# Optimization experiments

Measured on AMD Instinct MI355X. Metric: run time of the kernel, lower is better.

Reference implementation:

```python
import jax, jax.numpy as jnp
import numpy as np

B, T, D, K = 4, 2048, 1024, 4

def setup_inputs() -> dict:
    key = jax.random.key(0)
    ks = jax.random.split(key, 4)
    u = jax.random.normal(ks[0], (B, T, D), dtype=jnp.float32)
    s0 = jnp.zeros((B, K, D), dtype=jnp.float32)
    W_in = jax.random.normal(ks[1], (K * D, D), dtype=jnp.float32) * (1.0 / np.sqrt(D))
    b_in = jnp.zeros((K * D,), dtype=jnp.float32)
    W_out = jax.random.normal(ks[2], (D, K * D), dtype=jnp.float32) * (1.0 / np.sqrt(K * D))
    b_out = jnp.zeros((D,), dtype=jnp.float32)
    decay_logit = jax.random.normal(ks[3], (K,), dtype=jnp.float32)
    return {"u": u, "s0": s0, "W_in": W_in, "b_in": b_in,
            "W_out": W_out, "b_out": b_out, "decay_logit": decay_logit}

def reference(u, s0, W_in, b_in, W_out, b_out, decay_logit):
    # u: (B,T,D); s0: (B,K,D)
    Bb, Tt, Dd = u.shape
    Kk = decay_logit.shape[0]
    # input projection -> (B,T,K,D) -> (T,B,K,D) for scan over time
    inp = (jnp.einsum('btd,ed->bte', u, W_in) + b_in).reshape(Bb, Tt, Kk, Dd)
    xs = jnp.transpose(inp, (1, 0, 2, 3))  # (T,B,K,D)
    decay = jax.nn.sigmoid(decay_logit).reshape(1, Kk, 1)  # (1,K,1)

    def step(s, x):
        s_next = decay * s + x
        return s_next, s_next

    s_last, s_seq = jax.lax.scan(step, s0, xs)  # s_seq: (T,B,K,D)
    g_in = jnp.transpose(s_seq, (1, 0, 2, 3)).reshape(Bb, Tt, Kk * Dd)
    g = jnp.einsum('bte,de->btd', g_in, W_out) + b_out
    return g, s_last
```

## Files before the change

### kernel.cpp

```cpp
#include <hip/hip_runtime.h>


#define Bb 4
#define Tt 2048
#define Dd 1024
#define Kk 4
#define BT (Bb*Tt)
#define Ee (Kk*Dd)
#define NCH 32
#define LCH 64

typedef __bf16 bf16x8 __attribute__((ext_vector_type(8)));
typedef float  f32x4  __attribute__((ext_vector_type(4)));

__device__ __forceinline__ float bf2f(ushort u){
  union { unsigned int i; float f; } x; x.i = ((unsigned int)u) << 16; return x.f;
}
__device__ __forceinline__ ushort f2bf(float f){
  union { unsigned int i; float f; } x; x.f = f;
  unsigned int i = x.i;
  return (ushort)((i + 0x7FFFu + ((i >> 16) & 1u)) >> 16);
}
__device__ __forceinline__ float lo16(unsigned u){
  union { unsigned i; float f; } x; x.i = u << 16; return x.f;
}
__device__ __forceinline__ float hi16(unsigned u){
  union { unsigned i; float f; } x; x.i = u & 0xFFFF0000u; return x.f;
}
__device__ __forceinline__ float sigm(float x){ return 1.0f / (1.0f + expf(-x)); }

__global__ __launch_bounds__(256) void k_transpose(const float* __restrict__ in,
                                                   ushort* __restrict__ out){
  __shared__ float tile[32][33];
  int tx = threadIdx.x, ty = threadIdx.y;
  int c0 = blockIdx.x * 32, r0 = blockIdx.y * 32;
  #pragma unroll
  for (int j = 0; j < 4; ++j)
    tile[ty + j*8][tx] = in[(size_t)(r0 + ty + j*8) * Dd + c0 + tx];
  __syncthreads();
  #pragma unroll
  for (int j = 0; j < 4; ++j)
    out[(size_t)(c0 + ty + j*8) * Ee + r0 + tx] = f2bf(tile[tx][ty + j*8]);
}

__global__ __launch_bounds__(256) void k_wout(const float* __restrict__ Wout,
                                              const float* __restrict__ s0,
                                              const float* __restrict__ b_in,
                                              ushort* __restrict__ Wout_bf,
                                              float* __restrict__ z0,
                                              float* __restrict__ cterm){
  int gid  = blockIdx.x * 4 + (threadIdx.x >> 6);
  int lane = threadIdx.x & 63;
  int d = gid & 1023, k = gid >> 10;
  const float* wrow = Wout + (size_t)d * Ee + k * Dd;
  ushort*      wbf  = Wout_bf + (size_t)d * Ee + k * Dd;
  const float* bv   = b_in + k * Dd;
  float sc = 0.f, sz0 = 0.f, sz1 = 0.f, sz2 = 0.f, sz3 = 0.f;
  #pragma unroll
  for (int j = 0; j < 4; ++j){
    int base = lane*4 + j*256;
    float4 wv = *(const float4*)(wrow + base);
    ushort4 ob; ob.x = f2bf(wv.x); ob.y = f2bf(wv.y); ob.z = f2bf(wv.z); ob.w = f2bf(wv.w);
    *(ushort4*)(wbf + base) = ob;
    float4 bb = *(const float4*)(bv + base);
    sc += wv.x*bb.x + wv.y*bb.y + wv.z*bb.z + wv.w*bb.w;
    #pragma unroll
    for (int b = 0; b < 4; ++b){
      const float* sv = s0 + ((size_t)(b*Kk + k) << 10) + base;
      float4 s4 = *(const float4*)sv;
      float acc = wv.x*s4.x + wv.y*s4.y + wv.z*s4.z + wv.w*s4.w;
      if (b == 0) sz0 += acc; else if (b == 1) sz1 += acc;
      else if (b == 2) sz2 += acc; else sz3 += acc;
    }
  }
  for (int off = 32; off; off >>= 1){
    sc  += __shfl_down(sc, off);
    sz0 += __shfl_down(sz0, off);
    sz1 += __shfl_down(sz1, off);
    sz2 += __shfl_down(sz2, off);
    sz3 += __shfl_down(sz3, off);
  }
  if (lane == 0){
    cterm[gid] = sc;
    z0[gid]          = sz0;
    z0[gid + 4096]   = sz1;
    z0[gid + 8192]   = sz2;
    z0[gid + 12288]  = sz3;
  }
}

__global__ __launch_bounds__(256) void gemm_nt(const ushort* __restrict__ A,
                                               const ushort* __restrict__ B,
                                               ushort* __restrict__ C,
                                               int Kred, int lda, int ldb, int ldc,
                                               long aBatch, long bBatch, long cBatch){
  __shared__ ushort As[128 * 32];
  __shared__ ushort Bs[128 * 32];
  A += (long)blockIdx.z * aBatch;
  B += (long)blockIdx.z * bBatch;
  C += (long)blockIdx.z * cBatch;
  const int tid  = threadIdx.x;
  const int lane = tid & 63;
  const int w    = tid >> 6;
  const int wr   = w >> 1, wc = w & 1;
  const int rowBase = blockIdx.x * 128;
  const int colBase = blockIdx.y * 128;

  f32x4 acc[4][4] = {};
  const int krow = (lane >> 4) * 8;
  const int rsel = lane & 15;

  for (int kk = 0; kk < Kred; kk += 32){
    __syncthreads();
    #pragma unroll
    for (int i = 0; i < 2; ++i){
      int c  = i * 256 + tid;
      int r  = c >> 2;
      int c8 = (c & 3) * 8;
      const ushort* ga = A + (size_t)(rowBase + r) * lda + kk + c8;
      const ushort* gb = B + (size_t)(colBase + r) * ldb + kk + c8;
      __builtin_amdgcn_global_load_lds((const __attribute__((address_space(1))) void*)ga,
                                       (__attribute__((address_space(3))) void*)&As[c * 8],
                                       16, 0, 0);
      __builtin_amdgcn_global_load_lds((const __attribute__((address_space(1))) void*)gb,
                                       (__attribute__((address_space(3))) void*)&Bs[c * 8],
                                       16, 0, 0);
    }
    asm volatile("s_waitcnt vmcnt(0)" ::: "memory");
    __syncthreads();

    bf16x8 Af[4], Bf[4];
    #pragma unroll
    for (int mi = 0; mi < 4; ++mi)
      Af[mi] = *(const bf16x8*)&As[(wr*64 + mi*16 + rsel) * 32 + krow];
    #pragma unroll
    for (int ni = 0; ni < 4; ++ni)
      Bf[ni] = *(const bf16x8*)&Bs[(wc*64 + ni*16 + rsel) * 32 + krow];
    #pragma unroll
    for (int mi = 0; mi < 4; ++mi)
      #pragma unroll
      for (int ni = 0; ni < 4; ++ni)
        acc[mi][ni] = __builtin_amdgcn_mfma_f32_16x16x32_bf16(Af[mi], Bf[ni], acc[mi][ni], 0, 0, 0);
  }

  #pragma unroll
  for (int mi = 0; mi < 4; ++mi){
    #pragma unroll
    for (int ni = 0; ni < 4; ++ni){
      int r0 = rowBase + wr*64 + mi*16 + (lane >> 4) * 4;
      int c0 = colBase + wc*64 + ni*16 + (lane & 15);
      #pragma unroll
      for (int q = 0; q < 4; ++q)
        C[(size_t)(r0 + q) * ldc + c0] = f2bf(acc[mi][ni][q]);
    }
  }
}

#define STAGE_OP(GB, LOFF)                                                     \
  { _Pragma("unroll")                                                          \
    for (int i_ = 0; i_ < 2; ++i_){                                            \
      int c_ = tid + i_*256;                                                   \
      int row_ = c_ >> 2;                                                      \
      int ss_ = (c_ & 3) ^ ((row_ >> 1) & 3);                                  \
      const ushort* g_ = (GB) + (size_t)row_ * 1024 + ss_ * 8;                 \
      __builtin_amdgcn_global_load_lds(                                        \
        (const __attribute__((address_space(1))) void*)g_,                     \
        (__attribute__((address_space(3))) void*)&lds[(LOFF) + c_*8],          \
        16, 0, 0);                                                             \
    } }

#define LOAD_A4(DST)                                                           \
  { _Pragma("unroll")                                                          \
    for (int mi_ = 0; mi_ < 4; ++mi_){                                         \
      int r_ = wm*64 + mi_*16 + rsel;                                          \
      int uo_ = r_*32 + kq*8;                                                  \
      uo_ ^= ((uo_ >> 6) & 3) << 3;                                            \
      DST[mi_] = *(const bf16x8*)&lds[cbase + uo_];                            \
    } }

#define LOAD_B4(DST)                                                           \
  { _Pragma("unroll")                                                          \
    for (int ni_ = 0; ni_ < 4; ++ni_){                                         \
      int r_ = wn*64 + ni_*16 + rsel;                                          \
      int uo_ = r_*32 + kq*8;                                                  \
      uo_ ^= ((uo_ >> 6) & 3) << 3;                                            \
      DST[ni_] = *(const bf16x8*)&lds[cbase + 4096 + uo_];                     \
    } }

#define XB(R) ((((R) & 3) ^ (((R) >> 2) & 3)) << 5)
#define BAR() __builtin_amdgcn_s_barrier()

__global__ __launch_bounds__(256, 4) void gemm_big(const ushort* __restrict__ A,
                                                   const ushort* __restrict__ B,
                                                   ushort* __restrict__ C,
                                                   const float* __restrict__ dlog,
                                                   float* __restrict__ carry){
  __shared__ ushort lds[16384];
  const int tid  = threadIdx.x;
  const int lane = tid & 63;
  const int w    = tid >> 6;
  const int wm   = w >> 1;
  const int wn   = w & 1;
  const int rsel = lane & 15;
  const int kq   = lane >> 4;

  int bid = blockIdx.x;
  int xcd = bid & 7, rr = bid >> 3;
  const int rowBase = ((xcd >> 1) * 16 + (rr & 15)) * 128;
  const int colBase = ((xcd & 1) * 16 + (rr >> 4)) * 128;

  const ushort* Ag = A + (size_t)rowBase * 1024;
  const ushort* Bg = B + (size_t)colBase * 1024;

  f32x4 acc[4][4] = {};

  STAGE_OP(Ag +  0, 0);
  STAGE_OP(Bg +  0, 4096);
  STAGE_OP(Ag + 32, 8192);
  STAGE_OP(Bg + 32, 8192 + 4096);
  asm volatile("s_waitcnt vmcnt(4)" ::: "memory");
  BAR();

  for (int t = 0; t < 32; ++t){
    const int cbase = (t & 1) * 8192;
    bf16x8 af[4], bf[4];
    LOAD_A4(af); LOAD_B4(bf);
    #pragma unroll
    for (int mi = 0; mi < 4; ++mi)
      #pragma unroll
      for (int ni = 0; ni < 4; ++ni)
        acc[mi][ni] = __builtin_amdgcn_mfma_f32_16x16x32_bf16(af[mi], bf[ni], acc[mi][ni], 0, 0, 0);
    asm volatile("s_waitcnt lgkmcnt(0)" ::: "memory");
    BAR();
    if (t < 30){
      STAGE_OP(Ag + (t+2)*32, cbase);
      STAGE_OP(Bg + (t+2)*32, cbase + 4096);
      asm volatile("s_waitcnt vmcnt(4)" ::: "memory");
    } else {
      asm volatile("s_waitcnt vmcnt(0)" ::: "memory");
    }
    BAR();
  }

  #pragma unroll
  for (int mi = 0; mi < 4; ++mi){
    #pragma unroll
    for (int j = 0; j < 4; ++j){
      #pragma unroll
      for (int q = 0; q < 4; ++q){
        int row = wm*64 + mi*16 + (lane >> 4)*4 + q;
        int col = wn*64 + j*16 + rsel;
        int byte = (row*256 + col*2) ^ XB(row);
        *(ushort*)((char*)lds + byte) = f2bf(acc[mi][j][q]);
      }
    }
  }
  __syncthreads();

  if (tid < 128){
    const int k_blk = colBase >> 10;
    const int b_blk = rowBase >> 11;
    const int ch0   = (rowBase & 2047) >> 6;
    const int d0    = colBase & 1023;
    const float p   = sigm(dlog[k_blk]);
    int cp = tid & 63, ch = tid >> 6;
    float a0 = 0.f, a1 = 0.f;
    for (int i = 0; i < 64; ++i){
      int row = ch*64 + i;
      int byte = (row*256 + cp*4) ^ XB(row);
      unsigned v = *(const unsigned*)((char*)lds + byte);
      a0 = p * a0 + lo16(v);
      a1 = p * a1 + hi16(v);
    }
    float* cdst = &carry[(size_t)((b_blk*Kk + k_blk)*NCH + ch0 + ch) * Dd + d0 + cp*2];
    cdst[0] = a0; cdst[1] = a1;
  }

  #pragma unroll
  for (int j = 0; j < 8; ++j){
    int idx = tid + j*256;
    int r = idx >> 4, c16 = idx & 15;
    int byte = (r*256 + c16*16) ^ XB(r);
    f32x4 v = *(const f32x4*)((char*)lds + byte);
    *(f32x4*)&C[(size_t)(rowBase + r) * Ee + colBase + c16*8] = v;
  }
}

__global__ __launch_bounds__(256) void k_scanInc(const float* __restrict__ carry,
                                                 const float* __restrict__ z0,
                                                 const float* __restrict__ dlog,
                                                 float* __restrict__ incoming){
  int idx = blockIdx.x * 256 + threadIdx.x;
  int k = (idx >> 10) & 3;
  int bk = idx >> 10, d = idx & 1023;
  float p  = sigm(dlog[k]);
  float dL = powf(p, (float)LCH);
  float inc = z0[idx];
  for (int c = 0; c < NCH; ++c){
    size_t o = ((size_t)(bk * NCH + c)) * Dd + d;
    incoming[o] = inc;
    inc = dL * inc + carry[o];
  }
}

__global__ __launch_bounds__(256) void k_scanB(const ushort* __restrict__ Y,
                                               const float* __restrict__ incoming,
                                               const float* __restrict__ dlog,
                                               const float* __restrict__ b_out,
                                               const float* __restrict__ cterm,
                                               float* __restrict__ g){
  int x = blockIdx.x;
  int d = blockIdx.y * 256 + threadIdx.x;
  int c = x & 31, b = x >> 5;
  float p[4], z[4], ct[4], pw[4];
  #pragma unroll
  for (int k = 0; k < 4; ++k){
    p[k]  = sigm(dlog[k]);
    z[k]  = incoming[((size_t)(((b*Kk + k))*NCH + c)) * Dd + d];
    float omp = fmaxf(1.0f - p[k], 1e-30f);
    ct[k] = cterm[k * Dd + d] / omp;
    pw[k] = powf(p[k], (float)(c * LCH + 1));
  }
  float bo = b_out[d];
  size_t ybase = ((size_t)(b*Tt + c*LCH)) * Ee + d;
  size_t gbase = ((size_t)(b*Tt + c*LCH)) * Dd + d;
  for (int i = 0; i < LCH; ++i){
    float acc = bo;
    #pragma unroll
    for (int k = 0; k < 4; ++k){
      z[k] = p[k] * z[k] + bf2f(Y[ybase + (size_t)k * Dd]);
      acc += z[k] + ct[k] * (1.0f - pw[k]);
      pw[k] *= p[k];
    }
    g[gbase] = acc;
    ybase += Ee; gbase += Dd;
  }
}

__global__ __launch_bounds__(256) void k_prep(const float* __restrict__ u,
                                              const float* __restrict__ dlog,
                                              float* __restrict__ vpart,
                                              ushort* __restrict__ U_bf){
  int x = blockIdx.x;
  int d = blockIdx.y * 256 + threadIdx.x;
  int c = x & 31, b = x >> 5;
  float p[4], a[4] = {0.f, 0.f, 0.f, 0.f};
  #pragma unroll
  for (int k = 0; k < 4; ++k) p[k] = sigm(dlog[k]);
  size_t ub = ((size_t)(b*Tt + c*LCH)) * Dd + d;
  for (int i = 0; i < LCH; ++i){
    float uv = u[ub];
    U_bf[ub] = f2bf(uv);
    #pragma unroll
    for (int k = 0; k < 4; ++k) a[k] = p[k] * a[k] + uv;
    ub += Dd;
  }
  #pragma unroll
  for (int k = 0; k < 4; ++k)
    vpart[(((size_t)x) * Kk + k) * Dd + d] = a[k];
}

__global__ __launch_bounds__(256) void k_vcomb(const float* __restrict__ vpart,
                                               const float* __restrict__ dlog,
                                               float* __restrict__ vfull){
  int idx = blockIdx.x * 256 + threadIdx.x;
  int k = (idx >> 10) & 3, b = idx >> 12, d = idx & 1023;
  float p  = sigm(dlog[k]);
  float dL = powf(p, (float)LCH);
  float v = 0.f;
  for (int c = 0; c < NCH; ++c)
    v = dL * v + vpart[(((size_t)(b*NCH + c)) * Kk + k) * Dd + d];
  vfull[idx] = v;
}

__global__ __launch_bounds__(256) void k_slast(const float* __restrict__ W_in,
                                               const float* __restrict__ vfull,
                                               const float* __restrict__ s0,
                                               const float* __restrict__ b_in,
                                               const float* __restrict__ dlog,
                                               float* __restrict__ out){
  int gid  = blockIdx.x * 4 + (threadIdx.x >> 6);
  int lane = threadIdx.x & 63;
  int d = gid & 1023, k = (gid >> 10) & 3, b = gid >> 12;
  const float* wrow = W_in + (size_t)(k*Dd + d) * Dd;
  const float* vv   = vfull + ((size_t)(b*Kk + k) << 10);
  float s = 0.f;
  #pragma unroll
  for (int j = 0; j < 16; ++j) s += wrow[lane + j*64] * vv[lane + j*64];
  for (int off = 32; off; off >>= 1) s += __shfl_down(s, off);
  if (lane == 0){
    float p  = sigm(dlog[k]);
    float pT = powf(p, (float)Tt);
    float omp = 1.0f - p;
    float geo = (omp < 1e-12f) ? (float)Tt : (1.0f - pT) / omp;
    out[gid] = pT * s0[gid] + s + b_in[k*Dd + d] * geo;
  }
}

extern "C" void kernel_launch(void* const* d_in, const int* in_sizes, int n_in,
                              void* d_out, int out_size, void* d_ws, size_t ws_size,
                              hipStream_t stream){
  const float* u     = (const float*)d_in[0];
  const float* s0    = (const float*)d_in[1];
  const float* W_in  = (const float*)d_in[2];
  const float* b_in  = (const float*)d_in[3];
  const float* W_out = (const float*)d_in[4];
  const float* b_out = (const float*)d_in[5];
  const float* dlog  = (const float*)d_in[6];

  float* g_out     = (float*)d_out;
  float* slast_out = g_out + (size_t)BT * Dd;

  char* ws = (char*)d_ws;
  if (ws_size < 115490816ull) return;
  ushort* U_bf    = (ushort*)(ws);
  ushort* WinT    = (ushort*)(ws + 16777216);
  ushort* Wout_bf = (ushort*)(ws + 25165824);
  ushort* Mcat    = (ushort*)(ws + 33554432);
  ushort* Y       = (ushort*)(ws + 41943040);
  float*  carry   = (float*)(ws + 109051904);
  float*  incoming= (float*)(ws + 111149056);
  float*  z0buf   = (float*)(ws + 113246208);
  float*  cterm   = (float*)(ws + 113311744);
  float*  vpart   = (float*)(ws + 113328128);
  float*  vfull   = (float*)(ws + 115425280);

  k_prep<<<dim3(128, 4), 256, 0, stream>>>(u, dlog, vpart, U_bf);
  k_wout<<<1024, 256, 0, stream>>>(W_out, s0, b_in, Wout_bf, z0buf, cterm);
  k_transpose<<<dim3(32, 128), dim3(32, 8), 0, stream>>>(W_in, WinT);

  gemm_nt<<<dim3(8, 8, 4), 256, 0, stream>>>(Wout_bf, WinT, Mcat,
                                             1024, Ee, Ee, Dd,
                                             1024L, 1024L, 1048576L);
  gemm_big<<<2048, 256, 0, stream>>>(U_bf, Mcat, Y, dlog, carry);

  k_scanInc<<<64, 256, 0, stream>>>(carry, z0buf, dlog, incoming);
  k_scanB<<<dim3(128, 4), 256, 0, stream>>>(Y, incoming, dlog, b_out, cterm, g_out);

  k_vcomb<<<64, 256, 0, stream>>>(vpart, dlog, vfull);
  k_slast<<<4096, 256, 0, stream>>>(W_in, vfull, s0, b_in, dlog, slast_out);
}
```

Before: 167.3 us.

## Merge independent prep, scan and final kernels into fewer launches

Combines k_prep, k_wout and k_transpose into one kernel that picks its role from the block index. It likewise merges k_scanInc with k_vcomb, and k_scanB with k_slast. This cuts the number of kernel launches and lets independent work share the GPU at once. It also vectorizes the prep and scan loads and stores (f32x4 for u, two columns per thread with packed bf16 Y reads and float2 g writes, float4 in the s_last dot product). The cost is larger kernels whose branches can raise register pressure for every role.

```diff
diff --git a/kernel.cpp b/kernel.cpp
--- a/kernel.cpp
+++ b/kernel.cpp
@@ -29,63 +29,88 @@
 }
 __device__ __forceinline__ float sigm(float x){ return 1.0f / (1.0f + expf(-x)); }
 
-__global__ __launch_bounds__(256) void k_transpose(const float* __restrict__ in,
-                                                   ushort* __restrict__ out){
-  __shared__ float tile[32][33];
-  int tx = threadIdx.x, ty = threadIdx.y;
-  int c0 = blockIdx.x * 32, r0 = blockIdx.y * 32;
-  #pragma unroll
-  for (int j = 0; j < 4; ++j)
-    tile[ty + j*8][tx] = in[(size_t)(r0 + ty + j*8) * Dd + c0 + tx];
-  __syncthreads();
-  #pragma unroll
-  for (int j = 0; j < 4; ++j)
-    out[(size_t)(c0 + ty + j*8) * Ee + r0 + tx] = f2bf(tile[tx][ty + j*8]);
-}
-
-__global__ __launch_bounds__(256) void k_wout(const float* __restrict__ Wout,
-                                              const float* __restrict__ s0,
-                                              const float* __restrict__ b_in,
-                                              ushort* __restrict__ Wout_bf,
-                                              float* __restrict__ z0,
-                                              float* __restrict__ cterm){
-  int gid  = blockIdx.x * 4 + (threadIdx.x >> 6);
-  int lane = threadIdx.x & 63;
-  int d = gid & 1023, k = gid >> 10;
-  const float* wrow = Wout + (size_t)d * Ee + k * Dd;
-  ushort*      wbf  = Wout_bf + (size_t)d * Ee + k * Dd;
-  const float* bv   = b_in + k * Dd;
-  float sc = 0.f, sz0 = 0.f, sz1 = 0.f, sz2 = 0.f, sz3 = 0.f;
-  #pragma unroll
-  for (int j = 0; j < 4; ++j){
-    int base = lane*4 + j*256;
-    float4 wv = *(const float4*)(wrow + base);
-    ushort4 ob; ob.x = f2bf(wv.x); ob.y = f2bf(wv.y); ob.z = f2bf(wv.z); ob.w = f2bf(wv.w);
-    *(ushort4*)(wbf + base) = ob;
-    float4 bb = *(const float4*)(bv + base);
-    sc += wv.x*bb.x + wv.y*bb.y + wv.z*bb.z + wv.w*bb.w;
-    #pragma unroll
-    for (int b = 0; b < 4; ++b){
-      const float* sv = s0 + ((size_t)(b*Kk + k) << 10) + base;
-      float4 s4 = *(const float4*)sv;
-      float acc = wv.x*s4.x + wv.y*s4.y + wv.z*s4.z + wv.w*s4.w;
-      if (b == 0) sz0 += acc; else if (b == 1) sz1 += acc;
-      else if (b == 2) sz2 += acc; else sz3 += acc;
-    }
-  }
-  for (int off = 32; off; off >>= 1){
-    sc  += __shfl_down(sc, off);
-    sz0 += __shfl_down(sz0, off);
-    sz1 += __shfl_down(sz1, off);
-    sz2 += __shfl_down(sz2, off);
-    sz3 += __shfl_down(sz3, off);
-  }
-  if (lane == 0){
-    cterm[gid] = sc;
-    z0[gid]          = sz0;
-    z0[gid + 4096]   = sz1;
-    z0[gid + 8192]   = sz2;
-    z0[gid + 12288]  = sz3;
+__global__ __launch_bounds__(256) void k_prep_all(
+    const float* __restrict__ u, const float* __restrict__ dlog,
+    float* __restrict__ vpart, ushort* __restrict__ U_bf,
+    const float* __restrict__ W_in, ushort* __restrict__ WinT,
+    const float* __restrict__ Wout, const float* __restrict__ s0,
+    const float* __restrict__ b_in, ushort* __restrict__ Wout_bf,
+    float* __restrict__ z0, float* __restrict__ cterm){
+  const int bid = blockIdx.x;
+  const int tid = threadIdx.x;
+
+  if (bid < 128){
+    int x = bid, c = x & 31, b = x >> 5;
+    int d0 = tid * 4;
+    float p[4];
+    #pragma unroll
+    for (int k = 0; k < 4; ++k) p[k] = sigm(dlog[k]);
+    f32x4 a0 = {0,0,0,0}, a1 = {0,0,0,0}, a2 = {0,0,0,0}, a3 = {0,0,0,0};
+    size_t ub = ((size_t)(b*Tt + c*LCH)) * Dd + d0;
+    for (int i = 0; i < LCH; ++i){
+      f32x4 uv = *(const f32x4*)(u + ub);
+      ushort4 ob; ob.x = f2bf(uv[0]); ob.y = f2bf(uv[1]);
+      ob.z = f2bf(uv[2]); ob.w = f2bf(uv[3]);
+      *(ushort4*)(U_bf + ub) = ob;
+      a0 = p[0]*a0 + uv; a1 = p[1]*a1 + uv; a2 = p[2]*a2 + uv; a3 = p[3]*a3 + uv;
+      ub += Dd;
+    }
+    size_t vb = ((size_t)x * Kk) * Dd + d0;
+    *(f32x4*)(vpart + vb)          = a0;
+    *(f32x4*)(vpart + vb + Dd)     = a1;
+    *(f32x4*)(vpart + vb + 2*Dd)   = a2;
+    *(f32x4*)(vpart + vb + 3*Dd)   = a3;
+  } else if (bid < 4224){
+    __shared__ float tile[32][33];
+    int bb = bid - 128;
+    int c0 = (bb & 31) * 32, r0 = (bb >> 5) * 32;
+    int tx = tid & 31, ty = tid >> 5;
+    #pragma unroll
+    for (int j = 0; j < 4; ++j)
+      tile[ty + j*8][tx] = W_in[(size_t)(r0 + ty + j*8) * Dd + c0 + tx];
+    __syncthreads();
+    #pragma unroll
+    for (int j = 0; j < 4; ++j)
+      WinT[(size_t)(c0 + ty + j*8) * Ee + r0 + tx] = f2bf(tile[tx][ty + j*8]);
+  } else {
+    int gid  = (bid - 4224) * 4 + (tid >> 6);
+    int lane = tid & 63;
+    int d = gid & 1023, k = gid >> 10;
+    const float* wrow = Wout + (size_t)d * Ee + k * Dd;
+    ushort*      wbf  = Wout_bf + (size_t)d * Ee + k * Dd;
+    const float* bv   = b_in + k * Dd;
+    float sc = 0.f, sz0 = 0.f, sz1 = 0.f, sz2 = 0.f, sz3 = 0.f;
+    #pragma unroll
+    for (int j = 0; j < 4; ++j){
+      int base = lane*4 + j*256;
+      float4 wv = *(const float4*)(wrow + base);
+      ushort4 ob; ob.x = f2bf(wv.x); ob.y = f2bf(wv.y); ob.z = f2bf(wv.z); ob.w = f2bf(wv.w);
+      *(ushort4*)(wbf + base) = ob;
+      float4 bb4 = *(const float4*)(bv + base);
+      sc += wv.x*bb4.x + wv.y*bb4.y + wv.z*bb4.z + wv.w*bb4.w;
+      #pragma unroll
+      for (int b = 0; b < 4; ++b){
+        const float* sv = s0 + ((size_t)(b*Kk + k) << 10) + base;
+        float4 s4 = *(const float4*)sv;
+        float acc = wv.x*s4.x + wv.y*s4.y + wv.z*s4.z + wv.w*s4.w;
+        if (b == 0) sz0 += acc; else if (b == 1) sz1 += acc;
+        else if (b == 2) sz2 += acc; else sz3 += acc;
+      }
+    }
+    for (int off = 32; off; off >>= 1){
+      sc  += __shfl_down(sc, off);
+      sz0 += __shfl_down(sz0, off);
+      sz1 += __shfl_down(sz1, off);
+      sz2 += __shfl_down(sz2, off);
+      sz3 += __shfl_down(sz3, off);
+    }
+    if (lane == 0){
+      cterm[gid] = sc;
+      z0[gid]          = sz0;
+      z0[gid + 4096]   = sz1;
+      z0[gid + 8192]   = sz2;
+      z0[gid + 12288]  = sz3;
+    }
   }
 }
 
@@ -286,114 +311,106 @@
   }
 }
 
-__global__ __launch_bounds__(256) void k_scanInc(const float* __restrict__ carry,
-                                                 const float* __restrict__ z0,
-                                                 const float* __restrict__ dlog,
-                                                 float* __restrict__ incoming){
-  int idx = blockIdx.x * 256 + threadIdx.x;
-  int k = (idx >> 10) & 3;
-  int bk = idx >> 10, d = idx & 1023;
-  float p  = sigm(dlog[k]);
-  float dL = powf(p, (float)LCH);
-  float inc = z0[idx];
-  for (int c = 0; c < NCH; ++c){
-    size_t o = ((size_t)(bk * NCH + c)) * Dd + d;
-    incoming[o] = inc;
-    inc = dL * inc + carry[o];
-  }
-}
-
-__global__ __launch_bounds__(256) void k_scanB(const ushort* __restrict__ Y,
+__global__ __launch_bounds__(256) void k_mid(const float* __restrict__ carry,
+                                             const float* __restrict__ z0,
+                                             const float* __restrict__ dlog,
+                                             float* __restrict__ incoming,
+                                             const float* __restrict__ vpart,
+                                             float* __restrict__ vfull){
+  int bid = blockIdx.x, tid = threadIdx.x;
+  if (bid < 64){
+    int idx = bid * 256 + tid;
+    int k = (idx >> 10) & 3;
+    int bk = idx >> 10, d = idx & 1023;
+    float p  = sigm(dlog[k]);
+    float dL = powf(p, (float)LCH);
+    float inc = z0[idx];
+    for (int c = 0; c < NCH; ++c){
+      size_t o = ((size_t)(bk * NCH + c)) * Dd + d;
+      incoming[o] = inc;
+      inc = dL * inc + carry[o];
+    }
+  } else {
+    int idx = (bid - 64) * 256 + tid;
+    int k = (idx >> 10) & 3, b = idx >> 12, d = idx & 1023;
+    float p  = sigm(dlog[k]);
+    float dL = powf(p, (float)LCH);
+    float v = 0.f;
+    for (int c = 0; c < NCH; ++c)
+      v = dL * v + vpart[(((size_t)(b*NCH + c)) * Kk + k) * Dd + d];
+    vfull[idx] = v;
+  }
+}
+
+__global__ __launch_bounds__(256) void k_final(const ushort* __restrict__ Y,
                                                const float* __restrict__ incoming,
                                                const float* __restrict__ dlog,
                                                const float* __restrict__ b_out,
                                                const float* __restrict__ cterm,
-                                               float* __restrict__ g){
-  int x = blockIdx.x;
-  int d = blockIdx.y * 256 + threadIdx.x;
-  int c = x & 31, b = x >> 5;
-  float p[4], z[4], ct[4], pw[4];
-  #pragma unroll
-  for (int k = 0; k < 4; ++k){
-    p[k]  = sigm(dlog[k]);
-    z[k]  = incoming[((size_t)(((b*Kk + k))*NCH + c)) * Dd + d];
-    float omp = fmaxf(1.0f - p[k], 1e-30f);
-    ct[k] = cterm[k * Dd + d] / omp;
-    pw[k] = powf(p[k], (float)(c * LCH + 1));
-  }
-  float bo = b_out[d];
-  size_t ybase = ((size_t)(b*Tt + c*LCH)) * Ee + d;
-  size_t gbase = ((size_t)(b*Tt + c*LCH)) * Dd + d;
-  for (int i = 0; i < LCH; ++i){
-    float acc = bo;
-    #pragma unroll
-    for (int k = 0; k < 4; ++k){
-      z[k] = p[k] * z[k] + bf2f(Y[ybase + (size_t)k * Dd]);
-      acc += z[k] + ct[k] * (1.0f - pw[k]);
-      pw[k] *= p[k];
-    }
-    g[gbase] = acc;
-    ybase += Ee; gbase += Dd;
-  }
-}
-
-__global__ __launch_bounds__(256) void k_prep(const float* __restrict__ u,
-                                              const float* __restrict__ dlog,
-                                              float* __restrict__ vpart,
-                                              ushort* __restrict__ U_bf){
-  int x = blockIdx.x;
-  int d = blockIdx.y * 256 + threadIdx.x;
-  int c = x & 31, b = x >> 5;
-  float p[4], a[4] = {0.f, 0.f, 0.f, 0.f};
-  #pragma unroll
-  for (int k = 0; k < 4; ++k) p[k] = sigm(dlog[k]);
-  size_t ub = ((size_t)(b*Tt + c*LCH)) * Dd + d;
-  for (int i = 0; i < LCH; ++i){
-    float uv = u[ub];
-    U_bf[ub] = f2bf(uv);
-    #pragma unroll
-    for (int k = 0; k < 4; ++k) a[k] = p[k] * a[k] + uv;
-    ub += Dd;
-  }
-  #pragma unroll
-  for (int k = 0; k < 4; ++k)
-    vpart[(((size_t)x) * Kk + k) * Dd + d] = a[k];
-}
-
-__global__ __launch_bounds__(256) void k_vcomb(const float* __restrict__ vpart,
-                                               const float* __restrict__ dlog,
-                                               float* __restrict__ vfull){
-  int idx = blockIdx.x * 256 + threadIdx.x;
-  int k = (idx >> 10) & 3, b = idx >> 12, d = idx & 1023;
-  float p  = sigm(dlog[k]);
-  float dL = powf(p, (float)LCH);
-  float v = 0.f;
-  for (int c = 0; c < NCH; ++c)
-    v = dL * v + vpart[(((size_t)(b*NCH + c)) * Kk + k) * Dd + d];
-  vfull[idx] = v;
-}
-
-__global__ __launch_bounds__(256) void k_slast(const float* __restrict__ W_in,
+                                               float* __restrict__ g,
+                                               const float* __restrict__ W_in,
                                                const float* __restrict__ vfull,
                                                const float* __restrict__ s0,
                                                const float* __restrict__ b_in,
-                                               const float* __restrict__ dlog,
-                                               float* __restrict__ out){
-  int gid  = blockIdx.x * 4 + (threadIdx.x >> 6);
-  int lane = threadIdx.x & 63;
-  int d = gid & 1023, k = (gid >> 10) & 3, b = gid >> 12;
-  const float* wrow = W_in + (size_t)(k*Dd + d) * Dd;
-  const float* vv   = vfull + ((size_t)(b*Kk + k) << 10);
-  float s = 0.f;
-  #pragma unroll
-  for (int j = 0; j < 16; ++j) s += wrow[lane + j*64] * vv[lane + j*64];
-  for (int off = 32; off; off >>= 1) s += __shfl_down(s, off);
-  if (lane == 0){
-    float p  = sigm(dlog[k]);
-    float pT = powf(p, (float)Tt);
-    float omp = 1.0f - p;
-    float geo = (omp < 1e-12f) ? (float)Tt : (1.0f - pT) / omp;
-    out[gid] = pT * s0[gid] + s + b_in[k*Dd + d] * geo;
+                                               float* __restrict__ slast){
+  int bid = blockIdx.x, tid = threadIdx.x;
+  if (bid < 256){
+    int x = bid >> 1;
+    int c = x & 31, b = x >> 5;
+    int d = (bid & 1) * 512 + tid * 2;
+    float p[4], ct0[4], ct1[4], pw[4];
+    float z0v[4], z1v[4];
+    #pragma unroll
+    for (int k = 0; k < 4; ++k){
+      p[k]  = sigm(dlog[k]);
+      size_t io = ((size_t)(((b*Kk + k))*NCH + c)) * Dd + d;
+      z0v[k] = incoming[io];
+      z1v[k] = incoming[io + 1];
+      float omp = fmaxf(1.0f - p[k], 1e-30f);
+      ct0[k] = cterm[k * Dd + d] / omp;
+      ct1[k] = cterm[k * Dd + d + 1] / omp;
+      pw[k] = powf(p[k], (float)(c * LCH + 1));
+    }
+    float bo0 = b_out[d], bo1 = b_out[d + 1];
+    size_t ybase = ((size_t)(b*Tt + c*LCH)) * Ee + d;
+    size_t gbase = ((size_t)(b*Tt + c*LCH)) * Dd + d;
+    for (int i = 0; i < LCH; ++i){
+      float acc0 = bo0, acc1 = bo1;
+      #pragma unroll
+      for (int k = 0; k < 4; ++k){
+        unsigned yv = *(const unsigned*)&Y[ybase + (size_t)k * Dd];
+        z0v[k] = p[k] * z0v[k] + lo16(yv);
+        z1v[k] = p[k] * z1v[k] + hi16(yv);
+        float omw = 1.0f - pw[k];
+        acc0 += z0v[k] + ct0[k] * omw;
+        acc1 += z1v[k] + ct1[k] * omw;
+        pw[k] *= p[k];
+      }
+      *(float2*)&g[gbase] = make_float2(acc0, acc1);
+      ybase += Ee; gbase += Dd;
+    }
+  } else {
+    int gid  = (bid - 256) * 4 + (tid >> 6);
+    int lane = tid & 63;
+    int d = gid & 1023, k = (gid >> 10) & 3, b = gid >> 12;
+    const float* wrow = W_in + (size_t)(k*Dd + d) * Dd;
+    const float* vv   = vfull + ((size_t)(b*Kk + k) << 10);
+    float s = 0.f;
+    #pragma unroll
+    for (int j = 0; j < 4; ++j){
+      int base = lane*4 + j*256;
+      float4 w4 = *(const float4*)(wrow + base);
+      float4 v4 = *(const float4*)(vv + base);
+      s += w4.x*v4.x + w4.y*v4.y + w4.z*v4.z + w4.w*v4.w;
+    }
+    for (int off = 32; off; off >>= 1) s += __shfl_down(s, off);
+    if (lane == 0){
+      float p  = sigm(dlog[k]);
+      float pT = powf(p, (float)Tt);
+      float omp = 1.0f - p;
+      float geo = (omp < 1e-12f) ? (float)Tt : (1.0f - pT) / omp;
+      slast[gid] = pT * s0[gid] + s + b_in[k*Dd + d] * geo;
+    }
   }
 }
 
@@ -425,18 +442,17 @@
   float*  vpart   = (float*)(ws + 113328128);
   float*  vfull   = (float*)(ws + 115425280);
 
-  k_prep<<<dim3(128, 4), 256, 0, stream>>>(u, dlog, vpart, U_bf);
-  k_wout<<<1024, 256, 0, stream>>>(W_out, s0, b_in, Wout_bf, z0buf, cterm);
-  k_transpose<<<dim3(32, 128), dim3(32, 8), 0, stream>>>(W_in, WinT);
+  k_prep_all<<<5248, 256, 0, stream>>>(u, dlog, vpart, U_bf,
+                                       W_in, WinT,
+                                       W_out, s0, b_in, Wout_bf, z0buf, cterm);
 
   gemm_nt<<<dim3(8, 8, 4), 256, 0, stream>>>(Wout_bf, WinT, Mcat,
                                              1024, Ee, Ee, Dd,
                                              1024L, 1024L, 1048576L);
   gemm_big<<<2048, 256, 0, stream>>>(U_bf, Mcat, Y, dlog, carry);
 
-  k_scanInc<<<64, 256, 0, stream>>>(carry, z0buf, dlog, incoming);
-  k_scanB<<<dim3(128, 4), 256, 0, stream>>>(Y, incoming, dlog, b_out, cterm, g_out);
-
-  k_vcomb<<<64, 256, 0, stream>>>(vpart, dlog, vfull);
-  k_slast<<<4096, 256, 0, stream>>>(W_in, vfull, s0, b_in, dlog, slast_out);
-}
+  k_mid<<<128, 256, 0, stream>>>(carry, z0buf, dlog, incoming, vpart, vfull);
+
+  k_final<<<4352, 256, 0, stream>>>(Y, incoming, dlog, b_out, cterm, g_out,
+                                    W_in, vfull, s0, b_in, slast_out);
+}
```

Result: faster. 155.0 us (-7.4%).
